# Kernel tuning notes

Hardware: AMD Instinct MI355X
Metric: run time of the kernel (lower is better)

## Reference

```python
import jax, jax.numpy as jnp
import numpy as np

B, T, F, M = 32, 256, 512, 4   # batch, pred_len (=d_model=state_size), feature_dim (=mamba seq), time-mark feats
N = F - M                      # number of variates in x_enc
T2 = 2 * T
EPS = 1e-5


def setup_inputs() -> dict:
    key = jax.random.key(0)
    it = iter(jax.random.split(key, 32))
    def nrm(*s):
        return jax.random.normal(next(it), s, jnp.float32) * 0.02
    inp = {
        "x_enc": jax.random.normal(next(it), (B, T, N), jnp.float32),
        "x_mark_enc": jax.random.normal(next(it), (B, T, M), jnp.float32),
        "x_dec": jnp.zeros((1, 1, 1), jnp.float32),
        "x_mark_dec": jnp.zeros((1, 1, 1), jnp.float32),
        # 3 structurally identical MambaBlocks -> stack params on leading dim 3
        "norm_w": jnp.ones((3, T), jnp.float32),
        "inp_W": nrm(3, T, T2), "inp_b": jnp.zeros((3, T2), jnp.float32),
        "conv_W": nrm(3, F, F, 3), "conv_b": jnp.zeros((3, F), jnp.float32),
        "convlin_W": nrm(3, T2, T2), "convlin_b": jnp.zeros((3, T2), jnp.float32),
        "fc1_W": nrm(3, T2, T2), "fc1_b": jnp.zeros((3, T2), jnp.float32),
        "fc2_W": nrm(3, T2, T), "fc2_b": jnp.zeros((3, T), jnp.float32),
        "fc3_W": nrm(3, T2, T), "fc3_b": jnp.zeros((3, T), jnp.float32),
        "D_W": nrm(3, T, T2), "D_b": jnp.zeros((3, T2), jnp.float32),
        "out_W": nrm(3, T2, T), "out_b": jnp.ones((3, T), jnp.float32),  # out_proj.bias init to 1.0
        "proj_W": nrm(T, T), "proj_b": jnp.zeros((T,), jnp.float32),
    }
    return inp


def _rmsnorm(x, w):
    return x * jax.lax.rsqrt(jnp.mean(x * x, -1, keepdims=True) + EPS) * w


def _conv1d(x, W, b):
    # x: [B, C, L], W: [C_out, C_in, 3], padding=1
    y = jax.lax.conv_general_dilated(x, W, (1,), [(1, 1)], dimension_numbers=("NCH", "OIH", "NCH"))
    return y + b[None, :, None]


def _s6(x, fc1W, fc1b, fc2W, fc2b, fc3W, fc3b):
    # h is zero-initialized each call, so dA=exp(delta*A) multiplies zeros and
    # y = einsum('bln,bldn->bld', C, x[...,None]*dB) = delta * x * <C,B>_n
    Bmat = x @ fc2W + fc2b                         # [B, L, n]
    Cmat = x @ fc3W + fc3b                         # [B, L, n]
    delta = jax.nn.softplus(x @ fc1W + fc1b)       # [B, L, d]
    cb = jnp.einsum("bln,bln->bl", Cmat, Bmat)   # contraction over state dim
    return delta * x * cb[:, :, None]


def _block(x, i, p):
    xn = _rmsnorm(x, p["norm_w"][i])
    xp = xn @ p["inp_W"][i] + p["inp_b"][i]                      # [B, F, 2T]
    xc = jax.nn.silu(_conv1d(xp, p["conv_W"][i], p["conv_b"][i]))
    xco = xc @ p["convlin_W"][i] + p["convlin_b"][i]
    xssm = _s6(xco, p["fc1_W"][i], p["fc1_b"][i], p["fc2_W"][i], p["fc2_b"][i], p["fc3_W"][i], p["fc3_b"][i])
    xres = jax.nn.silu(xn @ p["D_W"][i] + p["D_b"][i])
    return (jax.nn.silu(xssm) * xres) @ p["out_W"][i] + p["out_b"][i]


def _forward(x_enc, x_mark_enc, p):
    means = jax.lax.stop_gradient(jnp.mean(x_enc, 1, keepdims=True))  # detached in torch
    xe = x_enc - means
    stdev = jnp.sqrt(jnp.var(xe, axis=1, keepdims=True) + 1e-5)       # NOT detached in torch
    xe = xe / stdev
    x = jnp.concatenate([xe, x_mark_enc], axis=2).transpose(0, 2, 1)  # [B, F, T]
    for i in range(3):
        x = _block(x, i, p)
    dec = (x @ p["proj_W"] + p["proj_b"]).transpose(0, 2, 1)          # [B, T, F]
    return dec[:, :, :N] * stdev + means                              # pred_len == T


def reference(x_enc, x_mark_enc, x_dec, x_mark_dec, norm_w, inp_W, inp_b, conv_W, conv_b, convlin_W, convlin_b, fc1_W, fc1_b, fc2_W, fc2_b, fc3_W, fc3_b, D_W, D_b, out_W, out_b, proj_W, proj_b):
    p = dict(norm_w=norm_w, inp_W=inp_W, inp_b=inp_b, conv_W=conv_W, conv_b=conv_b, convlin_W=convlin_W, convlin_b=convlin_b, fc1_W=fc1_W, fc1_b=fc1_b, fc2_W=fc2_W, fc2_b=fc2_b, fc3_W=fc3_W, fc3_b=fc3_b, D_W=D_W, D_b=D_b, out_W=out_W, out_b=out_b, proj_W=proj_W, proj_b=proj_b)
    return _forward(x_enc, x_mark_enc, p)
```

## Files before the change

kernel.cpp:

```cpp
#include <hip/hip_runtime.h>
#include <hip/hip_bf16.h>
#include <math.h>

typedef __hip_bfloat16 bf16;
typedef short short8 __attribute__((ext_vector_type(8)));
typedef short short4v __attribute__((ext_vector_type(4)));
typedef float floatx4 __attribute__((ext_vector_type(4)));

constexpr int CB_ = 32;
constexpr int CT = 256;
constexpr int CF = 512;
constexpr int CN = 508;
constexpr int CM = 4;
constexpr int CT2 = 512;
constexpr int MROWS = CB_ * CF;
constexpr int PADL = 528;

__device__ __forceinline__ float b2f(bf16 v) { return __bfloat162float(v); }
__device__ __forceinline__ bf16 f2b(float v) { return __float2bfloat16(v); }
__device__ __forceinline__ float s2f(short s) {
    unsigned u = ((unsigned)(unsigned short)s) << 16;
    return __builtin_bit_cast(float, u);
}
__device__ __forceinline__ short f2s(float v) {
    bf16 t = __float2bfloat16(v);
    return __builtin_bit_cast(short, t);
}
__device__ __forceinline__ float silu_f(float x) { return x / (1.0f + __expf(-x)); }
__device__ __forceinline__ float softplus_f(float x) {
    return fmaxf(x, 0.0f) + __logf(1.0f + __expf(-fabsf(x)));
}

__device__ __forceinline__ void gl_lds16(const bf16* g, short* l) {
    __builtin_amdgcn_global_load_lds(
        (const __attribute__((address_space(1))) unsigned int*)(g),
        (__attribute__((address_space(3))) unsigned int*)(l), 16, 0, 0);
}

struct P8 { const float* s[8]; bf16* d[8]; };
__global__ __launch_bounds__(256) void prepack_all_kernel(P8 p) {
    const int Ks[8]   = {256, 256, 512, 512, 512, 512, 512, 256};
    const int Ns[8]   = {512, 512, 512, 256, 256, 512, 256, 256};
    const int zs[8]   = {3, 3, 3, 3, 3, 3, 3, 1};
    const int dstr[8] = {262144, 262144, 524288, 524288, 524288, 262144, 131072, 65536};
    const int rml[8]  = {1, 1, 1, 2, 2, 1, 1, 1};
    const int rad[8]  = {0, 0, 0, 0, 1, 0, 0, 0};
    int bid = blockIdx.x;
    int m = 0, acc = 0;
    for (m = 0; m < 8; m++) {
        int c = (Ns[m] >> 5) * (Ks[m] >> 5) * zs[m];
        if (bid < acc + c) break;
        acc += c;
    }
    int lid = bid - acc;
    int K = Ks[m], N = Ns[m];
    int tx = N >> 5, ty = K >> 5;
    int z = lid / (tx * ty), rem = lid % (tx * ty);
    int k0 = (rem / tx) * 32, n0 = (rem % tx) * 32;
    const float* s = p.s[m] + (size_t)z * K * N;
    bf16* d = p.d[m] + (size_t)z * dstr[m];
    int mul = rml[m], add = rad[m];
    __shared__ float Ts[32][33];
    for (int e = threadIdx.x; e < 1024; e += 256) {
        int r = e >> 5, c = e & 31;
        Ts[r][c] = s[(size_t)(k0 + r) * N + n0 + c];
    }
    __syncthreads();
    for (int e = threadIdx.x; e < 1024; e += 256) {
        int r = e >> 5, c = e & 31;
        d[(size_t)((n0 + r) * mul + add) * K + k0 + c] = f2b(Ts[c][r]);
    }
}

constexpr int CONVN = 3 * 3 * 512 * 512;
__global__ void convpack_kernel(const float* __restrict__ src, bf16* __restrict__ dst,
                                bf16* __restrict__ xpT, float* __restrict__ CBv) {
    int idx = blockIdx.x * 256 + threadIdx.x;
    if (idx < CONVN) {
        int ci = idx & 511;
        int co = (idx >> 9) & 511;
        int it = idx >> 18;
        int tap = it % 3, ib = it / 3;
        dst[idx] = f2b(src[(((size_t)(ib * 512 + co)) * 512 + ci) * 3 + tap]);
    } else if (idx < CONVN + 32768) {
        int j = idx - CONVN;
        int ci = j & 511;
        int w = (j >> 9) & 1;
        int b = j >> 10;
        xpT[((size_t)b * PADL + (w ? 513 : 0)) * 512 + ci] = f2b(0.0f);
    } else if (idx < CONVN + 32768 + MROWS) {
        CBv[idx - CONVN - 32768] = 0.0f;
    }
}

__global__ __launch_bounds__(256) void buildx_rms_kernel(
    const float* __restrict__ xe, const float* __restrict__ xm,
    const float* __restrict__ nw, float* __restrict__ means, float* __restrict__ stdev,
    bf16* __restrict__ XN) {
    __shared__ float L[256][65];
    __shared__ float red_s[4][64], red_q[4][64];
    __shared__ float stat_m[64], stat_i[64], scl[64];
    int blk = blockIdx.x;
    int b = blk >> 3, f0 = (blk & 7) * 64;
    int tid = threadIdx.x;
    int j = tid & 63, tq = tid >> 6;
    int f = f0 + j;
    float ps = 0.f, pq = 0.f;
    const float* xep = xe + (size_t)b * CT * CN + f;
    const float* xmp = xm + (size_t)b * CT * CM + (f - CN);
    #pragma unroll 4
    for (int tt = 0; tt < 64; tt++) {
        int t = tq * 64 + tt;
        float v = (f < CN) ? xep[(size_t)t * CN] : xmp[(size_t)t * CM];
        L[t][j] = v;
        ps += v;
        pq += v * v;
    }
    red_s[tq][j] = ps;
    red_q[tq][j] = pq;
    __syncthreads();
    if (tid < 64) {
        int ff = f0 + tid;
        float s = red_s[0][tid] + red_s[1][tid] + red_s[2][tid] + red_s[3][tid];
        float q = red_q[0][tid] + red_q[1][tid] + red_q[2][tid] + red_q[3][tid];
        float mean, isd, msq;
        if (ff < CN) {
            mean = s * (1.0f / 256.0f);
            float var = fmaxf(q * (1.0f / 256.0f) - mean * mean, 0.0f);
            float sd = sqrtf(var + 1e-5f);
            isd = 1.0f / sd;
            means[b * CN + ff] = mean;
            stdev[b * CN + ff] = sd;
            msq = var / (var + 1e-5f);
        } else {
            mean = 0.0f;
            isd = 1.0f;
            msq = q * (1.0f / 256.0f);
        }
        stat_m[tid] = mean;
        stat_i[tid] = isd;
        scl[tid] = rsqrtf(msq + 1e-5f);
    }
    __syncthreads();
    bf16* outp = XN + ((size_t)(b * 512 + f0)) * 256;
    int t = tid;
    float w = nw[t];
    #pragma unroll 4
    for (int fp = 0; fp < 64; fp++) {
        float val = (L[t][fp] - stat_m[fp]) * stat_i[fp];
        outp[(size_t)fp * 256 + t] = f2b(val * scl[fp] * w);
    }
}

template <int MODE>
__global__ __launch_bounds__(256) void mgemm_kernel(const bf16* __restrict__ A,
                                                    const bf16* __restrict__ Wt,
                                                    const float* __restrict__ b1,
                                                    const float* __restrict__ b2,
                                                    bf16* __restrict__ o1,
                                                    bf16* __restrict__ o2,
                                                    int K, int Ncols) {
    __shared__ __align__(16) short As[128 * 32];
    __shared__ __align__(16) short Bs[128 * 32];
    const int tid = threadIdx.x;
    const int lane = tid & 63;
    const int wave = tid >> 6;
    const int m0 = blockIdx.x * 128, n0 = blockIdx.y * 128;

    const int srow0 = wave * 32;
    const int lrow = lane >> 2;
    const int lcol = (lane & 3) * 8;

    const bf16* aP0 = A + (size_t)(m0 + srow0 + lrow) * K + lcol;
    const bf16* aP1 = A + (size_t)(m0 + srow0 + 16 + lrow) * K + lcol;
    const bf16* bP0 = Wt + (size_t)(n0 + srow0 + lrow) * K + lcol;
    const bf16* bP1 = Wt + (size_t)(n0 + srow0 + 16 + lrow) * K + lcol;
    short* aL0 = &As[srow0 * 32];
    short* aL1 = &As[(srow0 + 16) * 32];
    short* bL0 = &Bs[srow0 * 32];
    short* bL1 = &Bs[(srow0 + 16) * 32];

    const int wm = (wave & 1) * 64, wn = (wave >> 1) * 64;
    const int fr = lane & 15, quad = lane >> 4;

    floatx4 acc[4][4];
    #pragma unroll
    for (int i = 0; i < 4; i++)
        #pragma unroll
        for (int j = 0; j < 4; j++) acc[i][j] = (floatx4){0.f, 0.f, 0.f, 0.f};

    for (int k0 = 0; k0 < K; k0 += 32) {
        gl_lds16(aP0 + k0, aL0);
        gl_lds16(aP1 + k0, aL1);
        gl_lds16(bP0 + k0, bL0);
        gl_lds16(bP1 + k0, bL1);
        __syncthreads();
        short8 af[4], bfv[4];
        #pragma unroll
        for (int i = 0; i < 4; i++) af[i] = *(const short8*)&As[(wm + i * 16 + fr) * 32 + quad * 8];
        #pragma unroll
        for (int j = 0; j < 4; j++) bfv[j] = *(const short8*)&Bs[(wn + j * 16 + fr) * 32 + quad * 8];
        #pragma unroll
        for (int i = 0; i < 4; i++)
            #pragma unroll
            for (int j = 0; j < 4; j++)
                acc[i][j] = __builtin_amdgcn_mfma_f32_16x16x32_bf16(af[i], bfv[j], acc[i][j], 0, 0, 0);
        __syncthreads();
    }

    if (MODE == 0) {
        #pragma unroll
        for (int j = 0; j < 4; j++) {
            int n = n0 + wn + j * 16 + fr;
            float bv = b1[n];
            #pragma unroll
            for (int i = 0; i < 4; i++) {
                int mb = m0 + wm + i * 16 + quad * 4;
                #pragma unroll
                for (int r = 0; r < 4; r++)
                    o1[(size_t)(mb + r) * Ncols + n] = f2b(acc[i][j][r] + bv);
            }
        }
    } else {
        if (n0 + wn < 512) {
            int b = (m0 + wm) >> 9;
            #pragma unroll
            for (int j = 0; j < 4; j++) {
                int n = n0 + wn + j * 16 + fr;
                float bv = b1[n];
                bf16* dst = o1 + ((size_t)b * PADL + n + 1) * 512;
                #pragma unroll
                for (int i = 0; i < 4; i++) {
                    int ci = (m0 + wm + i * 16 + quad * 4) & 511;
                    short4v pk;
                    #pragma unroll
                    for (int r = 0; r < 4; r++) pk[r] = f2s(acc[i][j][r] + bv);
                    *(short4v*)(dst + ci) = pk;
                }
            }
        } else {
            #pragma unroll
            for (int j = 0; j < 4; j++) {
                int n = n0 + wn + j * 16 + fr;
                float bv = b2[n - 512];
                #pragma unroll
                for (int i = 0; i < 4; i++) {
                    int mb = m0 + wm + i * 16 + quad * 4;
                    #pragma unroll
                    for (int r = 0; r < 4; r++)
                        o2[(size_t)(mb + r) * 512 + (n - 512)] = f2b(silu_f(acc[i][j][r] + bv));
                }
            }
        }
    }
}

__global__ __launch_bounds__(256) void cbgemm_kernel(const bf16* __restrict__ A,
                                                     const bf16* __restrict__ Wt,
                                                     const float* __restrict__ b2,
                                                     const float* __restrict__ b3,
                                                     float* __restrict__ CBv) {
    __shared__ __align__(16) short As[128 * 32];
    __shared__ __align__(16) short Bs[128 * 32];
    const int tid = threadIdx.x;
    const int lane = tid & 63;
    const int wave = tid >> 6;
    const int m0 = blockIdx.x * 128, n0 = blockIdx.y * 128;

    const int srow0 = wave * 32;
    const int lrow = lane >> 2;
    const int lcol = (lane & 3) * 8;
    const bf16* aP0 = A + (size_t)(m0 + srow0 + lrow) * 512 + lcol;
    const bf16* aP1 = A + (size_t)(m0 + srow0 + 16 + lrow) * 512 + lcol;
    const bf16* bP0 = Wt + (size_t)(n0 + srow0 + lrow) * 512 + lcol;
    const bf16* bP1 = Wt + (size_t)(n0 + srow0 + 16 + lrow) * 512 + lcol;
    short* aL0 = &As[srow0 * 32];
    short* aL1 = &As[(srow0 + 16) * 32];
    short* bL0 = &Bs[srow0 * 32];
    short* bL1 = &Bs[(srow0 + 16) * 32];

    const int wm = (wave & 1) * 64, wn = (wave >> 1) * 64;
    const int fr = lane & 15, quad = lane >> 4;

    floatx4 acc[4][4];
    #pragma unroll
    for (int i = 0; i < 4; i++)
        #pragma unroll
        for (int j = 0; j < 4; j++) acc[i][j] = (floatx4){0.f, 0.f, 0.f, 0.f};

    for (int k0 = 0; k0 < 512; k0 += 32) {
        gl_lds16(aP0 + k0, aL0);
        gl_lds16(aP1 + k0, aL1);
        gl_lds16(bP0 + k0, bL0);
        gl_lds16(bP1 + k0, bL1);
        __syncthreads();
        short8 af[4], bfv[4];
        #pragma unroll
        for (int i = 0; i < 4; i++) af[i] = *(const short8*)&As[(wm + i * 16 + fr) * 32 + quad * 8];
        #pragma unroll
        for (int j = 0; j < 4; j++) bfv[j] = *(const short8*)&Bs[(wn + j * 16 + fr) * 32 + quad * 8];
        #pragma unroll
        for (int i = 0; i < 4; i++)
            #pragma unroll
            for (int j = 0; j < 4; j++)
                acc[i][j] = __builtin_amdgcn_mfma_f32_16x16x32_bf16(af[i], bfv[j], acc[i][j], 0, 0, 0);
        __syncthreads();
    }
    int nnb = n0 + wn;
    float bv[4];
    #pragma unroll
    for (int j = 0; j < 4; j++) {
        int nn = nnb + j * 16 + fr;
        int c = nn >> 1;
        bv[j] = (fr & 1) ? b3[c] : b2[c];
    }
    #pragma unroll
    for (int i = 0; i < 4; i++) {
        #pragma unroll
        for (int r = 0; r < 4; r++) {
            float s = 0.f;
            #pragma unroll
            for (int j = 0; j < 4; j++) {
                float v = acc[i][j][r] + bv[j];
                s += v * __shfl_xor(v, 1);
            }
            s += __shfl_xor(s, 2);
            s += __shfl_xor(s, 4);
            s += __shfl_xor(s, 8);
            if (fr == 0)
                atomicAdd(&CBv[m0 + wm + i * 16 + quad * 4 + r], s * 0.5f);
        }
    }
}

__global__ __launch_bounds__(256) void fc1gate_kernel(const bf16* __restrict__ A,
                                                      const bf16* __restrict__ Wt,
                                                      const float* __restrict__ b1,
                                                      const float* __restrict__ CBv,
                                                      const bf16* __restrict__ Xres,
                                                      bf16* __restrict__ G) {
    __shared__ __align__(16) short As[128 * 32];
    __shared__ __align__(16) short Bs[128 * 32];
    const int tid = threadIdx.x;
    const int lane = tid & 63;
    const int wave = tid >> 6;
    const int m0 = blockIdx.x * 128, n0 = blockIdx.y * 128;

    const int srow0 = wave * 32;
    const int lrow = lane >> 2;
    const int lcol = (lane & 3) * 8;
    const bf16* aP0 = A + (size_t)(m0 + srow0 + lrow) * 512 + lcol;
    const bf16* aP1 = A + (size_t)(m0 + srow0 + 16 + lrow) * 512 + lcol;
    const bf16* bP0 = Wt + (size_t)(n0 + srow0 + lrow) * 512 + lcol;
    const bf16* bP1 = Wt + (size_t)(n0 + srow0 + 16 + lrow) * 512 + lcol;
    short* aL0 = &As[srow0 * 32];
    short* aL1 = &As[(srow0 + 16) * 32];
    short* bL0 = &Bs[srow0 * 32];
    short* bL1 = &Bs[(srow0 + 16) * 32];

    const int wm = (wave & 1) * 64, wn = (wave >> 1) * 64;
    const int fr = lane & 15, quad = lane >> 4;

    floatx4 acc[4][4];
    #pragma unroll
    for (int i = 0; i < 4; i++)
        #pragma unroll
        for (int j = 0; j < 4; j++) acc[i][j] = (floatx4){0.f, 0.f, 0.f, 0.f};

    for (int k0 = 0; k0 < 512; k0 += 32) {
        gl_lds16(aP0 + k0, aL0);
        gl_lds16(aP1 + k0, aL1);
        gl_lds16(bP0 + k0, bL0);
        gl_lds16(bP1 + k0, bL1);
        __syncthreads();
        short8 af[4], bfv[4];
        #pragma unroll
        for (int i = 0; i < 4; i++) af[i] = *(const short8*)&As[(wm + i * 16 + fr) * 32 + quad * 8];
        #pragma unroll
        for (int j = 0; j < 4; j++) bfv[j] = *(const short8*)&Bs[(wn + j * 16 + fr) * 32 + quad * 8];
        #pragma unroll
        for (int i = 0; i < 4; i++)
            #pragma unroll
            for (int j = 0; j < 4; j++)
                acc[i][j] = __builtin_amdgcn_mfma_f32_16x16x32_bf16(af[i], bfv[j], acc[i][j], 0, 0, 0);
        __syncthreads();
    }
    #pragma unroll
    for (int i = 0; i < 4; i++) {
        int mb = m0 + wm + i * 16 + quad * 4;
        float cbr[4];
        #pragma unroll
        for (int r = 0; r < 4; r++) cbr[r] = CBv[mb + r];
        #pragma unroll
        for (int j = 0; j < 4; j++) {
            int n = n0 + wn + j * 16 + fr;
            float bv = b1[n];
            #pragma unroll
            for (int r = 0; r < 4; r++) {
                size_t off = (size_t)(mb + r) * 512 + n;
                float delta = softplus_f(acc[i][j][r] + bv);
                float xssm = delta * b2f(A[off]) * cbr[r];
                G[off] = f2b(silu_f(xssm) * b2f(Xres[off]));
            }
        }
    }
}

__global__ __launch_bounds__(256) void conv_mfma_kernel(const bf16* __restrict__ Wc,
                                                        const bf16* __restrict__ xpT,
                                                        const float* __restrict__ bias,
                                                        bf16* __restrict__ Out,
                                                        float* __restrict__ CBvZ) {
    __shared__ __align__(16) short As[3 * 128 * 32];
    __shared__ __align__(16) short Bs[144 * 32];
    const int tid = threadIdx.x;
    const int lane = tid & 63;
    const int wave = tid >> 6;
    int bx = blockIdx.x;
    if (bx < 128 && tid < 128) CBvZ[bx * 128 + tid] = 0.0f;
    int xcd = bx & 7, g = bx >> 3;
    int mt = g & 3;
    int id = xcd * 16 + (g >> 2);
    int nt = id & 3, b = id >> 2;
    const int m0 = mt * 128, n0 = nt * 128;
    const bf16* xb = xpT + (size_t)b * PADL * 512;

    const int lrow = lane >> 2;
    const int lcol = (lane & 3) * 8;
    const int wm = (wave & 1) * 64, wn = (wave >> 1) * 64;
    const int fr = lane & 15, quad = lane >> 4;

    floatx4 acc[4][4];
    #pragma unroll
    for (int i = 0; i < 4; i++)
        #pragma unroll
        for (int j = 0; j < 4; j++) acc[i][j] = (floatx4){0.f, 0.f, 0.f, 0.f};

    for (int k0 = 0; k0 < 512; k0 += 32) {
        for (int ga = wave; ga < 24; ga += 4) {
            int tap = ga >> 3, rg = ga & 7;
            gl_lds16(Wc + (size_t)tap * 262144 + (size_t)(m0 + rg * 16 + lrow) * 512 + k0 + lcol,
                     &As[ga * 512]);
        }
        for (int gb = wave; gb < 9; gb += 4) {
            gl_lds16(xb + (size_t)(n0 + gb * 16 + lrow) * 512 + k0 + lcol, &Bs[gb * 512]);
        }
        __syncthreads();
        #pragma unroll
        for (int tap = 0; tap < 3; tap++) {
            short8 af[4], bfv[4];
            #pragma unroll
            for (int i = 0; i < 4; i++)
                af[i] = *(const short8*)&As[tap * 4096 + (wm + i * 16 + fr) * 32 + quad * 8];
            #pragma unroll
            for (int j = 0; j < 4; j++)
                bfv[j] = *(const short8*)&Bs[(wn + j * 16 + fr + tap) * 32 + quad * 8];
            #pragma unroll
            for (int i = 0; i < 4; i++)
                #pragma unroll
                for (int j = 0; j < 4; j++)
                    acc[i][j] = __builtin_amdgcn_mfma_f32_16x16x32_bf16(af[i], bfv[j], acc[i][j], 0, 0, 0);
        }
        __syncthreads();
    }
    bf16* ob = Out + (size_t)b * CF * CT2;
    #pragma unroll
    for (int i = 0; i < 4; i++) {
        int mb = m0 + wm + i * 16 + quad * 4;
        #pragma unroll
        for (int r = 0; r < 4; r++) {
            float bv = bias[mb + r];
            #pragma unroll
            for (int j = 0; j < 4; j++) {
                int n = n0 + wn + j * 16 + fr;
                ob[(size_t)(mb + r) * CT2 + n] = f2b(silu_f(acc[i][j][r] + bv));
            }
        }
    }
}

__global__ __launch_bounds__(256) void gemm_rms_kernel(const bf16* __restrict__ A,
                                                       const bf16* __restrict__ Wt,
                                                       const float* __restrict__ bias,
                                                       const float* __restrict__ nw,
                                                       bf16* __restrict__ Xo,
                                                       bf16* __restrict__ XNo) {
    __shared__ __align__(16) short As[64 * 32];
    __shared__ __align__(16) short Bs[256 * 32];
    __shared__ float red[4][64];
    __shared__ float scl[64];
    const int tid = threadIdx.x;
    const int lane = tid & 63;
    const int wave = tid >> 6;
    const int m0 = blockIdx.x * 64;

    const int lrow = lane >> 2;
    const int lcol = (lane & 3) * 8;
    const bf16* aP = A + (size_t)(m0 + wave * 16 + lrow) * 512 + lcol;
    short* aL = &As[wave * 16 * 32];
    const bf16* bP[4];
    short* bL[4];
    #pragma unroll
    for (int g = 0; g < 4; g++) {
        int r0 = (wave * 4 + g) * 16;
        bP[g] = Wt + (size_t)(r0 + lrow) * 512 + lcol;
        bL[g] = &Bs[r0 * 32];
    }
    const int wn = wave * 64;
    const int fr = lane & 15, quad = lane >> 4;

    floatx4 acc[4][4];
    #pragma unroll
    for (int i = 0; i < 4; i++)
        #pragma unroll
        for (int j = 0; j < 4; j++) acc[i][j] = (floatx4){0.f, 0.f, 0.f, 0.f};

    for (int k0 = 0; k0 < 512; k0 += 32) {
        gl_lds16(aP + k0, aL);
        #pragma unroll
        for (int g = 0; g < 4; g++) gl_lds16(bP[g] + k0, bL[g]);
        __syncthreads();
        short8 af[4], bfv[4];
        #pragma unroll
        for (int i = 0; i < 4; i++) af[i] = *(const short8*)&As[(i * 16 + fr) * 32 + quad * 8];
        #pragma unroll
        for (int j = 0; j < 4; j++) bfv[j] = *(const short8*)&Bs[(wn + j * 16 + fr) * 32 + quad * 8];
        #pragma unroll
        for (int i = 0; i < 4; i++)
            #pragma unroll
            for (int j = 0; j < 4; j++)
                acc[i][j] = __builtin_amdgcn_mfma_f32_16x16x32_bf16(af[i], bfv[j], acc[i][j], 0, 0, 0);
        __syncthreads();
    }
    #pragma unroll
    for (int j = 0; j < 4; j++) {
        float bv = bias[wn + j * 16 + fr];
        #pragma unroll
        for (int i = 0; i < 4; i++)
            #pragma unroll
            for (int r = 0; r < 4; r++) acc[i][j][r] += bv;
    }
    #pragma unroll
    for (int i = 0; i < 4; i++) {
        #pragma unroll
        for (int r = 0; r < 4; r++) {
            float s = 0.f;
            #pragma unroll
            for (int j = 0; j < 4; j++) s += acc[i][j][r] * acc[i][j][r];
            #pragma unroll
            for (int o = 8; o > 0; o >>= 1) s += __shfl_xor(s, o);
            if (fr == 0) red[wave][i * 16 + quad * 4 + r] = s;
        }
    }
    __syncthreads();
    if (tid < 64) {
        float tot = red[0][tid] + red[1][tid] + red[2][tid] + red[3][tid];
        scl[tid] = rsqrtf(tot * (1.0f / CT) + 1e-5f);
    }
    __syncthreads();
    #pragma unroll
    for (int j = 0; j < 4; j++) {
        int n = wn + j * 16 + fr;
        float w = nw[n];
        #pragma unroll
        for (int i = 0; i < 4; i++) {
            int rl = i * 16 + quad * 4;
            #pragma unroll
            for (int r = 0; r < 4; r++) {
                float v = acc[i][j][r];
                Xo[(size_t)(m0 + rl + r) * CT + n] = f2b(v);
                XNo[(size_t)(m0 + rl + r) * CT + n] = f2b(v * scl[rl + r] * w);
            }
        }
    }
}

__global__ __launch_bounds__(256) void proj_out_kernel(const bf16* __restrict__ A,
                                                       const bf16* __restrict__ Wt,
                                                       const float* __restrict__ bias,
                                                       const float* __restrict__ means,
                                                       const float* __restrict__ stdev,
                                                       float* __restrict__ out) {
    __shared__ __align__(16) short As[128 * 32];
    __shared__ __align__(16) short Bs[128 * 32];
    const int tid = threadIdx.x;
    const int lane = tid & 63;
    const int wave = tid >> 6;
    const int m0 = blockIdx.x * 128, n0 = blockIdx.y * 128;

    const int srow0 = wave * 32;
    const int lrow = lane >> 2;
    const int lcol = (lane & 3) * 8;
    const bf16* aP0 = A + (size_t)(m0 + srow0 + lrow) * 256 + lcol;
    const bf16* aP1 = A + (size_t)(m0 + srow0 + 16 + lrow) * 256 + lcol;
    const bf16* bP0 = Wt + (size_t)(n0 + srow0 + lrow) * 256 + lcol;
    const bf16* bP1 = Wt + (size_t)(n0 + srow0 + 16 + lrow) * 256 + lcol;
    short* aL0 = &As[srow0 * 32];
    short* aL1 = &As[(srow0 + 16) * 32];
    short* bL0 = &Bs[srow0 * 32];
    short* bL1 = &Bs[(srow0 + 16) * 32];

    const int wm = (wave & 1) * 64, wn = (wave >> 1) * 64;
    const int fr = lane & 15, quad = lane >> 4;

    floatx4 acc[4][4];
    #pragma unroll
    for (int i = 0; i < 4; i++)
        #pragma unroll
        for (int j = 0; j < 4; j++) acc[i][j] = (floatx4){0.f, 0.f, 0.f, 0.f};

    for (int k0 = 0; k0 < 256; k0 += 32) {
        gl_lds16(aP0 + k0, aL0);
        gl_lds16(aP1 + k0, aL1);
        gl_lds16(bP0 + k0, bL0);
        gl_lds16(bP1 + k0, bL1);
        __syncthreads();
        short8 af[4], bfv[4];
        #pragma unroll
        for (int i = 0; i < 4; i++) af[i] = *(const short8*)&As[(wm + i * 16 + fr) * 32 + quad * 8];
        #pragma unroll
        for (int j = 0; j < 4; j++) bfv[j] = *(const short8*)&Bs[(wn + j * 16 + fr) * 32 + quad * 8];
        #pragma unroll
        for (int i = 0; i < 4; i++)
            #pragma unroll
            for (int j = 0; j < 4; j++)
                acc[i][j] = __builtin_amdgcn_mfma_f32_16x16x32_bf16(af[i], bfv[j], acc[i][j], 0, 0, 0);
        __syncthreads();
    }
    #pragma unroll
    for (int j = 0; j < 4; j++) {
        int t = n0 + wn + j * 16 + fr;
        float bv = bias[t];
        #pragma unroll
        for (int i = 0; i < 4; i++) {
            int mb = m0 + wm + i * 16 + quad * 4;
            int b = mb >> 9;
            int nv = mb & 511;
            if (nv < CN) {
                floatx4 o;
                #pragma unroll
                for (int r = 0; r < 4; r++) {
                    int sn = b * CN + nv + r;
                    o[r] = (acc[i][j][r] + bv) * stdev[sn] + means[sn];
                }
                *(floatx4*)(out + ((size_t)(b * CT + t)) * CN + nv) = o;
            }
        }
    }
}

extern "C" void kernel_launch(void* const* d_in, const int* in_sizes, int n_in,
                              void* d_out, int out_size, void* d_ws, size_t ws_size,
                              hipStream_t stream) {
    const float* x_enc  = (const float*)d_in[0];
    const float* x_mark = (const float*)d_in[1];
    const float* norm_w = (const float*)d_in[4];
    const float* inp_W  = (const float*)d_in[5];
    const float* inp_b  = (const float*)d_in[6];
    const float* conv_W = (const float*)d_in[7];
    const float* conv_b = (const float*)d_in[8];
    const float* convlin_W = (const float*)d_in[9];
    const float* convlin_b = (const float*)d_in[10];
    const float* fc1_W = (const float*)d_in[11];
    const float* fc1_b = (const float*)d_in[12];
    const float* fc2_W = (const float*)d_in[13];
    const float* fc2_b = (const float*)d_in[14];
    const float* fc3_W = (const float*)d_in[15];
    const float* fc3_b = (const float*)d_in[16];
    const float* D_W   = (const float*)d_in[17];
    const float* D_b   = (const float*)d_in[18];
    const float* out_W = (const float*)d_in[19];
    const float* out_b = (const float*)d_in[20];
    const float* proj_W = (const float*)d_in[21];
    const float* proj_b = (const float*)d_in[22];

    char* ws = (char*)d_ws;
    float* MEANS = (float*)(ws);
    float* STDEV = (float*)(ws + 65536);
    float* CBv   = (float*)(ws + 131072);
    bf16* wt = (bf16*)(ws + 196608);
    bf16* wt_g1      = wt;
    bf16* wt_g3      = wt + 786432;
    bf16* wt_convlin = wt + 2359296;
    bf16* wt_out     = wt + 3145728;
    bf16* wt_proj    = wt + 3538944;
    bf16* wt_conv    = wt + 3604480;
    bf16* xpT = (bf16*)(ws + 12124160);
    const size_t POOLB = 16777216;
    const size_t HALF = 16384 * 256;
    bf16* pool[4] = {
        (bf16*)(ws + 29425664),
        (bf16*)(ws + 29425664 + POOLB),
        (bf16*)(ws + 29425664 + 2 * POOLB),
        (bf16*)(ws + 29425664 + 3 * POOLB),
    };
    float* out = (float*)d_out;

    P8 p;
    p.s[0] = inp_W;  p.d[0] = wt_g1;
    p.s[1] = D_W;    p.d[1] = wt_g1 + 131072;
    p.s[2] = fc1_W;  p.d[2] = wt_g3;
    p.s[3] = fc2_W;  p.d[3] = wt_g3 + 262144;
    p.s[4] = fc3_W;  p.d[4] = wt_g3 + 262144;
    p.s[5] = convlin_W; p.d[5] = wt_convlin;
    p.s[6] = out_W;  p.d[6] = wt_out;
    p.s[7] = proj_W; p.d[7] = wt_proj;
    prepack_all_kernel<<<3520, 256, 0, stream>>>(p);
    convpack_kernel<<<(CONVN + 32768 + MROWS + 255) / 256, 256, 0, stream>>>(
        conv_W, wt_conv, xpT, CBv);

    buildx_rms_kernel<<<256, 256, 0, stream>>>(x_enc, x_mark, norm_w, MEANS, STDEV,
                                               pool[0] + HALF);

    int ia = 0, ico = 1, ires = 2, iout = 3;
    for (int i = 0; i < 3; i++) {
        bf16* A  = pool[ia];
        bf16* XCO = pool[ico];
        bf16* XRES = pool[ires];
        bf16* OUTP = pool[iout];
        bf16* XN = A + HALF;

        mgemm_kernel<1><<<dim3(128, 8), 256, 0, stream>>>(
            XN, wt_g1 + (size_t)i * 262144, inp_b + i * CT2, D_b + i * CT2,
            xpT, XRES, 256, 1024);
        conv_mfma_kernel<<<512, 256, 0, stream>>>(wt_conv + (size_t)i * 786432, xpT,
                                                  conv_b + i * CF, A, CBv);
        mgemm_kernel<0><<<dim3(128, 4), 256, 0, stream>>>(
            A, wt_convlin + (size_t)i * 262144, convlin_b + i * CT2, nullptr,
            XCO, nullptr, 512, 512);
        cbgemm_kernel<<<dim3(128, 4), 256, 0, stream>>>(
            XCO, wt_g3 + (size_t)i * 524288 + 262144, fc2_b + i * CT, fc3_b + i * CT, CBv);
        fc1gate_kernel<<<dim3(128, 4), 256, 0, stream>>>(
            XCO, wt_g3 + (size_t)i * 524288, fc1_b + i * CT2, CBv, XRES, A);
        gemm_rms_kernel<<<256, 256, 0, stream>>>(
            A, wt_out + (size_t)i * 131072, out_b + i * CT,
            norm_w + ((i + 1) % 3) * CT, OUTP, OUTP + HALF);

        int na = iout, nco = ia, nres = ico, nout = ires;
        ia = na; ico = nco; ires = nres; iout = nout;
    }

    proj_out_kernel<<<dim3(128, 2), 256, 0, stream>>>(
        pool[ia], wt_proj, proj_b, MEANS, STDEV, out);
}
```

Measured before the change: 569.9 us.

## Fold RMSNorm weight into packed weights and apply row scale in GEMM epilogue

The RMSNorm weight is multiplied into the packed inp/D weight matrices at prepack time. The per-row rsqrt scale is stored as a float vector and applied in the epilogue of the following GEMM. This removes the separately written normalized activation copy (XN) in buildx and in the out-proj GEMM, cutting one bf16 store per element per block. The conv-pack kernel is also merged into the prepack launch to save one launch. The tradeoff is an extra scale load per row in the mgemm epilogue, and bf16 rounding now happens before scaling rather than after.

```diff
diff --git a/kernel.cpp b/kernel.cpp
--- a/kernel.cpp
+++ b/kernel.cpp
@@ -37,15 +37,40 @@
         (__attribute__((address_space(3))) unsigned int*)(l), 16, 0, 0);
 }
 
+constexpr int CONVN = 3 * 3 * 512 * 512;
+constexpr int MTILES = 3520;
 struct P8 { const float* s[8]; bf16* d[8]; };
-__global__ __launch_bounds__(256) void prepack_all_kernel(P8 p) {
+__global__ __launch_bounds__(256) void prepack_all_kernel(P8 p, const float* __restrict__ nw,
+                                                          const float* __restrict__ convW,
+                                                          bf16* __restrict__ convD,
+                                                          bf16* __restrict__ xpT,
+                                                          float* __restrict__ CBv) {
+    int bid = blockIdx.x;
+    if (bid >= MTILES) {
+        int idx = (bid - MTILES) * 256 + threadIdx.x;
+        if (idx < CONVN) {
+            int ci = idx & 511;
+            int co = (idx >> 9) & 511;
+            int it = idx >> 18;
+            int tap = it % 3, ib = it / 3;
+            convD[idx] = f2b(convW[(((size_t)(ib * 512 + co)) * 512 + ci) * 3 + tap]);
+        } else if (idx < CONVN + 32768) {
+            int j = idx - CONVN;
+            int ci = j & 511;
+            int w = (j >> 9) & 1;
+            int b = j >> 10;
+            xpT[((size_t)b * PADL + (w ? 513 : 0)) * 512 + ci] = f2b(0.0f);
+        } else if (idx < CONVN + 32768 + MROWS) {
+            CBv[idx - CONVN - 32768] = 0.0f;
+        }
+        return;
+    }
     const int Ks[8]   = {256, 256, 512, 512, 512, 512, 512, 256};
     const int Ns[8]   = {512, 512, 512, 256, 256, 512, 256, 256};
     const int zs[8]   = {3, 3, 3, 3, 3, 3, 3, 1};
     const int dstr[8] = {262144, 262144, 524288, 524288, 524288, 262144, 131072, 65536};
     const int rml[8]  = {1, 1, 1, 2, 2, 1, 1, 1};
     const int rad[8]  = {0, 0, 0, 0, 1, 0, 0, 0};
-    int bid = blockIdx.x;
     int m = 0, acc = 0;
     for (m = 0; m < 8; m++) {
         int c = (Ns[m] >> 5) * (Ks[m] >> 5) * zs[m];
@@ -60,10 +85,13 @@
     const float* s = p.s[m] + (size_t)z * K * N;
     bf16* d = p.d[m] + (size_t)z * dstr[m];
     int mul = rml[m], add = rad[m];
+    bool fold = (m <= 1);
     __shared__ float Ts[32][33];
     for (int e = threadIdx.x; e < 1024; e += 256) {
         int r = e >> 5, c = e & 31;
-        Ts[r][c] = s[(size_t)(k0 + r) * N + n0 + c];
+        float v = s[(size_t)(k0 + r) * N + n0 + c];
+        if (fold) v *= nw[z * 256 + k0 + r];
+        Ts[r][c] = v;
     }
     __syncthreads();
     for (int e = threadIdx.x; e < 1024; e += 256) {
@@ -72,34 +100,13 @@
     }
 }
 
-constexpr int CONVN = 3 * 3 * 512 * 512;
-__global__ void convpack_kernel(const float* __restrict__ src, bf16* __restrict__ dst,
-                                bf16* __restrict__ xpT, float* __restrict__ CBv) {
-    int idx = blockIdx.x * 256 + threadIdx.x;
-    if (idx < CONVN) {
-        int ci = idx & 511;
-        int co = (idx >> 9) & 511;
-        int it = idx >> 18;
-        int tap = it % 3, ib = it / 3;
-        dst[idx] = f2b(src[(((size_t)(ib * 512 + co)) * 512 + ci) * 3 + tap]);
-    } else if (idx < CONVN + 32768) {
-        int j = idx - CONVN;
-        int ci = j & 511;
-        int w = (j >> 9) & 1;
-        int b = j >> 10;
-        xpT[((size_t)b * PADL + (w ? 513 : 0)) * 512 + ci] = f2b(0.0f);
-    } else if (idx < CONVN + 32768 + MROWS) {
-        CBv[idx - CONVN - 32768] = 0.0f;
-    }
-}
-
-__global__ __launch_bounds__(256) void buildx_rms_kernel(
+__global__ __launch_bounds__(256) void buildx_kernel(
     const float* __restrict__ xe, const float* __restrict__ xm,
-    const float* __restrict__ nw, float* __restrict__ means, float* __restrict__ stdev,
-    bf16* __restrict__ XN) {
+    float* __restrict__ means, float* __restrict__ stdev,
+    bf16* __restrict__ X0, float* __restrict__ SCL) {
     __shared__ float L[256][65];
     __shared__ float red_s[4][64], red_q[4][64];
-    __shared__ float stat_m[64], stat_i[64], scl[64];
+    __shared__ float stat_m[64], stat_i[64];
     int blk = blockIdx.x;
     int b = blk >> 3, f0 = (blk & 7) * 64;
     int tid = threadIdx.x;
@@ -139,16 +146,15 @@
         }
         stat_m[tid] = mean;
         stat_i[tid] = isd;
-        scl[tid] = rsqrtf(msq + 1e-5f);
+        SCL[b * 512 + ff] = rsqrtf(msq + 1e-5f);
     }
     __syncthreads();
-    bf16* outp = XN + ((size_t)(b * 512 + f0)) * 256;
+    bf16* outp = X0 + ((size_t)(b * 512 + f0)) * 256;
     int t = tid;
-    float w = nw[t];
     #pragma unroll 4
     for (int fp = 0; fp < 64; fp++) {
         float val = (L[t][fp] - stat_m[fp]) * stat_i[fp];
-        outp[(size_t)fp * 256 + t] = f2b(val * scl[fp] * w);
+        outp[(size_t)fp * 256 + t] = f2b(val);
     }
 }
 
@@ -157,6 +163,7 @@
                                                     const bf16* __restrict__ Wt,
                                                     const float* __restrict__ b1,
                                                     const float* __restrict__ b2,
+                                                    const float* __restrict__ SCL,
                                                     bf16* __restrict__ o1,
                                                     bf16* __restrict__ o2,
                                                     int K, int Ncols) {
@@ -225,30 +232,38 @@
         if (n0 + wn < 512) {
             int b = (m0 + wm) >> 9;
             #pragma unroll
-            for (int j = 0; j < 4; j++) {
-                int n = n0 + wn + j * 16 + fr;
-                float bv = b1[n];
-                bf16* dst = o1 + ((size_t)b * PADL + n + 1) * 512;
+            for (int i = 0; i < 4; i++) {
+                int mb = m0 + wm + i * 16 + quad * 4;
+                float sclr[4];
                 #pragma unroll
-                for (int i = 0; i < 4; i++) {
-                    int ci = (m0 + wm + i * 16 + quad * 4) & 511;
+                for (int r = 0; r < 4; r++) sclr[r] = SCL[mb + r];
+                #pragma unroll
+                for (int j = 0; j < 4; j++) {
+                    int n = n0 + wn + j * 16 + fr;
+                    float bv = b1[n];
+                    bf16* dst = o1 + ((size_t)b * PADL + n + 1) * 512;
+                    int ci = mb & 511;
                     short4v pk;
                     #pragma unroll
-                    for (int r = 0; r < 4; r++) pk[r] = f2s(acc[i][j][r] + bv);
+                    for (int r = 0; r < 4; r++) pk[r] = f2s(acc[i][j][r] * sclr[r] + bv);
                     *(short4v*)(dst + ci) = pk;
                 }
             }
         } else {
             #pragma unroll
-            for (int j = 0; j < 4; j++) {
-                int n = n0 + wn + j * 16 + fr;
-                float bv = b2[n - 512];
+            for (int i = 0; i < 4; i++) {
+                int mb = m0 + wm + i * 16 + quad * 4;
+                float sclr[4];
                 #pragma unroll
-                for (int i = 0; i < 4; i++) {
-                    int mb = m0 + wm + i * 16 + quad * 4;
+                for (int r = 0; r < 4; r++) sclr[r] = SCL[mb + r];
+                #pragma unroll
+                for (int j = 0; j < 4; j++) {
+                    int n = n0 + wn + j * 16 + fr;
+                    float bv = b2[n - 512];
                     #pragma unroll
                     for (int r = 0; r < 4; r++)
-                        o2[(size_t)(mb + r) * 512 + (n - 512)] = f2b(silu_f(acc[i][j][r] + bv));
+                        o2[(size_t)(mb + r) * 512 + (n - 512)] =
+                            f2b(silu_f(acc[i][j][r] * sclr[r] + bv));
                 }
             }
         }
@@ -479,16 +494,14 @@
     }
 }
 
-__global__ __launch_bounds__(256) void gemm_rms_kernel(const bf16* __restrict__ A,
+__global__ __launch_bounds__(256) void gemm_scl_kernel(const bf16* __restrict__ A,
                                                        const bf16* __restrict__ Wt,
                                                        const float* __restrict__ bias,
-                                                       const float* __restrict__ nw,
                                                        bf16* __restrict__ Xo,
-                                                       bf16* __restrict__ XNo) {
+                                                       float* __restrict__ SCL) {
     __shared__ __align__(16) short As[64 * 32];
     __shared__ __align__(16) short Bs[256 * 32];
     __shared__ float red[4][64];
-    __shared__ float scl[64];
     const int tid = threadIdx.x;
     const int lane = tid & 63;
     const int wave = tid >> 6;
@@ -555,22 +568,17 @@
     __syncthreads();
     if (tid < 64) {
         float tot = red[0][tid] + red[1][tid] + red[2][tid] + red[3][tid];
-        scl[tid] = rsqrtf(tot * (1.0f / CT) + 1e-5f);
-    }
-    __syncthreads();
+        SCL[m0 + tid] = rsqrtf(tot * (1.0f / CT) + 1e-5f);
+    }
     #pragma unroll
     for (int j = 0; j < 4; j++) {
         int n = wn + j * 16 + fr;
-        float w = nw[n];
         #pragma unroll
         for (int i = 0; i < 4; i++) {
             int rl = i * 16 + quad * 4;
             #pragma unroll
-            for (int r = 0; r < 4; r++) {
-                float v = acc[i][j][r];
-                Xo[(size_t)(m0 + rl + r) * CT + n] = f2b(v);
-                XNo[(size_t)(m0 + rl + r) * CT + n] = f2b(v * scl[rl + r] * w);
-            }
+            for (int r = 0; r < 4; r++)
+                Xo[(size_t)(m0 + rl + r) * CT + n] = f2b(acc[i][j][r]);
         }
     }
 }
@@ -678,21 +686,21 @@
     float* MEANS = (float*)(ws);
     float* STDEV = (float*)(ws + 65536);
     float* CBv   = (float*)(ws + 131072);
-    bf16* wt = (bf16*)(ws + 196608);
+    float* SCL   = (float*)(ws + 196608);
+    bf16* wt = (bf16*)(ws + 262144);
     bf16* wt_g1      = wt;
     bf16* wt_g3      = wt + 786432;
     bf16* wt_convlin = wt + 2359296;
     bf16* wt_out     = wt + 3145728;
     bf16* wt_proj    = wt + 3538944;
     bf16* wt_conv    = wt + 3604480;
-    bf16* xpT = (bf16*)(ws + 12124160);
+    bf16* xpT = (bf16*)(ws + 12189696);
     const size_t POOLB = 16777216;
-    const size_t HALF = 16384 * 256;
     bf16* pool[4] = {
-        (bf16*)(ws + 29425664),
-        (bf16*)(ws + 29425664 + POOLB),
-        (bf16*)(ws + 29425664 + 2 * POOLB),
-        (bf16*)(ws + 29425664 + 3 * POOLB),
+        (bf16*)(ws + 29491200),
+        (bf16*)(ws + 29491200 + POOLB),
+        (bf16*)(ws + 29491200 + 2 * POOLB),
+        (bf16*)(ws + 29491200 + 3 * POOLB),
     };
     float* out = (float*)d_out;
 
@@ -705,12 +713,11 @@
     p.s[5] = convlin_W; p.d[5] = wt_convlin;
     p.s[6] = out_W;  p.d[6] = wt_out;
     p.s[7] = proj_W; p.d[7] = wt_proj;
-    prepack_all_kernel<<<3520, 256, 0, stream>>>(p);
-    convpack_kernel<<<(CONVN + 32768 + MROWS + 255) / 256, 256, 0, stream>>>(
-        conv_W, wt_conv, xpT, CBv);
-
-    buildx_rms_kernel<<<256, 256, 0, stream>>>(x_enc, x_mark, norm_w, MEANS, STDEV,
-                                               pool[0] + HALF);
+    int convBlocks = (CONVN + 32768 + MROWS + 255) / 256;
+    prepack_all_kernel<<<MTILES + convBlocks, 256, 0, stream>>>(
+        p, norm_w, conv_W, wt_conv, xpT, CBv);
+
+    buildx_kernel<<<256, 256, 0, stream>>>(x_enc, x_mark, MEANS, STDEV, pool[0], SCL);
 
     int ia = 0, ico = 1, ires = 2, iout = 3;
     for (int i = 0; i < 3; i++) {
@@ -718,23 +725,21 @@
         bf16* XCO = pool[ico];
         bf16* XRES = pool[ires];
         bf16* OUTP = pool[iout];
-        bf16* XN = A + HALF;
 
         mgemm_kernel<1><<<dim3(128, 8), 256, 0, stream>>>(
-            XN, wt_g1 + (size_t)i * 262144, inp_b + i * CT2, D_b + i * CT2,
+            A, wt_g1 + (size_t)i * 262144, inp_b + i * CT2, D_b + i * CT2, SCL,
             xpT, XRES, 256, 1024);
         conv_mfma_kernel<<<512, 256, 0, stream>>>(wt_conv + (size_t)i * 786432, xpT,
                                                   conv_b + i * CF, A, CBv);
         mgemm_kernel<0><<<dim3(128, 4), 256, 0, stream>>>(
-            A, wt_convlin + (size_t)i * 262144, convlin_b + i * CT2, nullptr,
+            A, wt_convlin + (size_t)i * 262144, convlin_b + i * CT2, nullptr, nullptr,
             XCO, nullptr, 512, 512);
         cbgemm_kernel<<<dim3(128, 4), 256, 0, stream>>>(
             XCO, wt_g3 + (size_t)i * 524288 + 262144, fc2_b + i * CT, fc3_b + i * CT, CBv);
         fc1gate_kernel<<<dim3(128, 4), 256, 0, stream>>>(
             XCO, wt_g3 + (size_t)i * 524288, fc1_b + i * CT2, CBv, XRES, A);
-        gemm_rms_kernel<<<256, 256, 0, stream>>>(
-            A, wt_out + (size_t)i * 131072, out_b + i * CT,
-            norm_w + ((i + 1) % 3) * CT, OUTP, OUTP + HALF);
+        gemm_scl_kernel<<<256, 256, 0, stream>>>(
+            A, wt_out + (size_t)i * 131072, out_b + i * CT, OUTP, SCL);
 
         int na = iout, nco = ia, nres = ico, nout = ires;
         ia = na; ico = nco; ires = nres; iout = nout;
```

After: 556.1 us. 1.02x faster.
